# Performance work log

Hardware: AMD Instinct MI355X
Metric: run time of the kernel (lower is better)

The kernel has to match this reference:

```python
import jax, jax.numpy as jnp
import numpy as np

B, S, D, V = 256, 128, 768, 30522
MASK_ID = 103
# vocab ids of the label words (8 positive, 6 neutral, 7 negative)
LABEL_IDS = [
    [2307, 2204, 3835, 2157, 6581, 2986, 5151, 3893],
    [7929, 24791, 8699, 4257, 16021, 6623],
    [6659, 2919, 11771, 3532, 11325, 4997, 13135],
]


def setup_inputs() -> dict:
    key = jax.random.key(0)
    ks = jax.random.split(key, 12)
    length = jax.random.randint(ks[0], (B,), 5, 105)          # 3+length <= 108 < S
    input_ids = jax.random.randint(ks[1], (B, S), 200, 30000)  # never hits MASK_ID
    input_ids = input_ids.at[jnp.arange(B), 3 + length].set(MASK_ID)  # one [MASK] per row
    bert_out = jax.random.normal(ks[2], (B, S, D), dtype=jnp.float32)
    p = lambda k, shp: 0.02 * jax.random.normal(k, shp, dtype=jnp.float32)
    return {
        'bert_out': bert_out,
        'input_ids': input_ids,
        'length': length,
        'senti_w': p(ks[3], (2, D)), 'senti_b': p(ks[4], (2,)),
        'dense_w': p(ks[5], (D, 2 * D)), 'dense_b': p(ks[6], (D,)),
        'dec_w': p(ks[7], (V, D)), 'dec_b': p(ks[8], (V,)),
        'w0': p(ks[9], (2, 8)), 'w1': p(ks[10], (2, 6)), 'w2': p(ks[11], (2, 7)),
    }


def reference(bert_out, input_ids, length, senti_w, senti_b, dense_w, dense_b,
              dec_w, dec_b, w0, w1, w2):
    # pooler -> sentiment head (Dropout is identity at inference)
    pooler = bert_out[:, 0]                                   # [B, D]
    category_out = pooler @ senti_w.T + senti_b               # [B, 2]

    # per-row [MASK] hidden state (exactly one MASK_ID per row)
    mask_pos = jnp.argmax(input_ids == MASK_ID, axis=1)       # [B]
    mask_logits = jnp.take_along_axis(bert_out, mask_pos[:, None, None], axis=1)[:, 0]  # [B, D]

    # attention(): softmax over the ragged slice bert_out[i, 3:3+length[i]]
    scores_raw = jnp.einsum('bsd,bd->bs', bert_out, mask_logits)        # [B, S]
    idx = jnp.arange(S)
    valid = (idx[None, :] >= 3) & (idx[None, :] < 3 + length[:, None])  # [B, S]
    scores = jax.nn.softmax(jnp.where(valid, scores_raw, -jnp.inf), axis=1)
    scores = jnp.where(valid, scores, 0.0)
    att = jnp.einsum('bs,bsd->bd', scores, bert_out)          # [B, D]

    feats = jnp.concatenate([att, mask_logits], axis=1)       # [B, 2D]
    h = jnp.tanh(feats @ dense_w.T + dense_b)                 # [B, D]
    probs = jnp.tanh(h @ dec_w.T + dec_b)                     # [B, V]

    outs = []
    for ids, w in zip(LABEL_IDS, (w0, w1, w2)):
        lp = probs[:, jnp.array(ids)]                         # [B, k]
        outs.append(lp @ w.T)                                 # [B, 2]
    out = jnp.stack(outs, axis=2)                             # [B, 2, 3]
    return category_out, out
```

## Files before the change

kernel.cpp:

```cpp
#include <hip/hip_runtime.h>
#include <hip/hip_bf16.h>
#include <math.h>

#define BB 256
#define SS 128
#define DD 768
#define K2 1536
#define MASK_ID 103

typedef __attribute__((ext_vector_type(8))) short short8;
typedef __attribute__((ext_vector_type(4))) float floatx4;

__constant__ int c_ids[21] = {
    2307, 2204, 3835, 2157, 6581, 2986, 5151, 3893,
    7929, 24791, 8699, 4257, 16021, 6623,
    6659, 2919, 11771, 3532, 11325, 4997, 13135
};

__device__ __forceinline__ float waveReduceSum(float v) {
    #pragma unroll
    for (int off = 32; off > 0; off >>= 1) v += __shfl_down(v, off, 64);
    return v;
}
__device__ __forceinline__ float waveReduceMax(float v) {
    #pragma unroll
    for (int off = 32; off > 0; off >>= 1) v = fmaxf(v, __shfl_down(v, off, 64));
    return v;
}
__device__ __forceinline__ unsigned short f2bf(float f) {
    unsigned int u = __float_as_uint(f);
    u += 0x7FFF + ((u >> 16) & 1);
    return (unsigned short)(u >> 16);
}

__global__ __launch_bounds__(256) void k_cvt(
    const float* __restrict__ src, unsigned short* __restrict__ dst, int n4)
{
    int i = blockIdx.x * 256 + threadIdx.x;
    if (i < n4) {
        float4 v = ((const float4*)src)[i];
        ushort4 o;
        o.x = f2bf(v.x); o.y = f2bf(v.y); o.z = f2bf(v.z); o.w = f2bf(v.w);
        ((ushort4*)dst)[i] = o;
    }
}

__global__ __launch_bounds__(512) void k_att(
    const float* __restrict__ bert, const int* __restrict__ ids,
    const int* __restrict__ len, const float* __restrict__ senti_w,
    const float* __restrict__ senti_b, float* __restrict__ cat_out,
    unsigned short* __restrict__ feats)
{
    __shared__ __align__(16) float s_mask[DD];
    __shared__ __align__(16) float s_part[8][DD];
    __shared__ float s_sc[SS];
    __shared__ float s_red[16];
    __shared__ int s_mp;

    const int b = blockIdx.x;
    const int tid = threadIdx.x;
    const int lane = tid & 63;
    const int wave = tid >> 6;

    if (tid == 0) s_mp = SS;
    __syncthreads();
    if (tid < SS && ids[b * SS + tid] == MASK_ID) atomicMin(&s_mp, tid);
    __syncthreads();
    const int mp = (s_mp == SS) ? 0 : s_mp;
    const int L = len[b];
    const float* base = bert + (size_t)b * SS * DD;
    const float* mrow = base + (size_t)mp * DD;

    float c0 = 0.f, c1 = 0.f;
    for (int d = tid; d < DD; d += 512) {
        s_mask[d] = mrow[d];
        float x = base[d];
        c0 += x * senti_w[d];
        c1 += x * senti_w[DD + d];
    }
    c0 = waveReduceSum(c0);
    c1 = waveReduceSum(c1);
    if (lane == 0) { s_red[wave] = c0; s_red[8 + wave] = c1; }
    __syncthreads();
    if (tid == 0) {
        float t0 = 0.f, t1 = 0.f;
        #pragma unroll
        for (int w = 0; w < 8; ++w) { t0 += s_red[w]; t1 += s_red[8 + w]; }
        cat_out[b * 2 + 0] = t0 + senti_b[0];
        cat_out[b * 2 + 1] = t1 + senti_b[1];
    }

    const float4* m4 = (const float4*)s_mask;
    for (int s = 3 + wave; s < 3 + L; s += 8) {
        const float4* row = (const float4*)(base + (size_t)s * DD);
        float acc = 0.f;
        #pragma unroll
        for (int i = 0; i < 3; ++i) {
            float4 r = row[lane + 64 * i];
            float4 mm = m4[lane + 64 * i];
            acc += r.x * mm.x + r.y * mm.y + r.z * mm.z + r.w * mm.w;
        }
        acc = waveReduceSum(acc);
        if (lane == 0) s_sc[s] = acc;
    }
    __syncthreads();

    const bool valid = (tid >= 3 && tid < 3 + L);
    float v = valid ? s_sc[tid] : -INFINITY;
    float mx = waveReduceMax(v);
    __syncthreads();
    if (lane == 0) s_red[wave] = mx;
    __syncthreads();
    float bm = s_red[0];
    #pragma unroll
    for (int w = 1; w < 8; ++w) bm = fmaxf(bm, s_red[w]);
    float e = valid ? expf(v - bm) : 0.f;
    float ssum = waveReduceSum(e);
    __syncthreads();
    if (lane == 0) s_red[wave] = ssum;
    __syncthreads();
    float tot = 0.f;
    #pragma unroll
    for (int w = 0; w < 8; ++w) tot += s_red[w];
    if (tid < SS) s_sc[tid] = e / tot;
    __syncthreads();

    float4 a0 = {0,0,0,0}, a1 = {0,0,0,0}, a2 = {0,0,0,0};
    for (int s = 3 + wave; s < 3 + L; s += 8) {
        const float w = s_sc[s];
        const float4* row = (const float4*)(base + (size_t)s * DD);
        float4 r0 = row[lane], r1 = row[lane + 64], r2 = row[lane + 128];
        a0.x += w * r0.x; a0.y += w * r0.y; a0.z += w * r0.z; a0.w += w * r0.w;
        a1.x += w * r1.x; a1.y += w * r1.y; a1.z += w * r1.z; a1.w += w * r1.w;
        a2.x += w * r2.x; a2.y += w * r2.y; a2.z += w * r2.z; a2.w += w * r2.w;
    }
    float4* pw = (float4*)s_part[wave];
    pw[lane] = a0; pw[lane + 64] = a1; pw[lane + 128] = a2;
    __syncthreads();

    unsigned short* fb = feats + (size_t)b * K2;
    for (int d = tid; d < DD; d += 512) {
        float a = 0.f;
        #pragma unroll
        for (int w = 0; w < 8; ++w) a += s_part[w][d];
        fb[d] = f2bf(a);
        fb[DD + d] = f2bf(s_mask[d]);
    }
}

__global__ __launch_bounds__(256) void k_dense(
    const unsigned short* __restrict__ featsb,
    const unsigned short* __restrict__ dwb,
    const float* __restrict__ db, float* __restrict__ h)
{
    const int tid = threadIdx.x;
    const int lane = tid & 63, wave = tid >> 6;
    const int b0 = blockIdx.y * 32 + (wave >> 1) * 16;
    const int j0 = blockIdx.x * 32 + (wave & 1) * 16;
    const int m = lane & 15, q = lane >> 4;

    const short8* Arow = (const short8*)(featsb + (size_t)(b0 + m) * K2);
    const short8* Brow = (const short8*)(dwb + (size_t)(j0 + m) * K2);
    floatx4 acc = {0.f, 0.f, 0.f, 0.f};
    #pragma unroll 8
    for (int k8 = 0; k8 < K2 / 8; k8 += 4) {
        short8 a = Arow[k8 + q];
        short8 w = Brow[k8 + q];
        acc = __builtin_amdgcn_mfma_f32_16x16x32_bf16(a, w, acc, 0, 0, 0);
    }
    const int col = j0 + m;
    const int rb = b0 + q * 4;
    const float bias = db[col];
    #pragma unroll
    for (int r = 0; r < 4; ++r)
        h[(size_t)(rb + r) * DD + col] = tanhf(acc[r] + bias);
}

__global__ __launch_bounds__(256) void k_dec(
    const float* __restrict__ h, const float* __restrict__ dec_w,
    const float* __restrict__ dec_b, const float* __restrict__ w0,
    const float* __restrict__ w1, const float* __restrict__ w2,
    float* __restrict__ out)
{
    __shared__ __align__(16) float s_h[DD];
    __shared__ float s_p[21];
    const int b = blockIdx.x;
    const int tid = threadIdx.x;
    const int lane = tid & 63, wave = tid >> 6;

    for (int d = tid; d < DD; d += 256) s_h[d] = h[(size_t)b * DD + d];
    __syncthreads();

    for (int idx = wave; idx < 21; idx += 4) {
        const int vid = c_ids[idx];
        const float* wr = dec_w + (size_t)vid * DD;
        float acc = 0.f;
        #pragma unroll
        for (int i = 0; i < DD / 64; ++i)
            acc += s_h[lane + 64 * i] * wr[lane + 64 * i];
        acc = waveReduceSum(acc);
        if (lane == 0) s_p[idx] = tanhf(acc + dec_b[vid]);
    }
    __syncthreads();

    if (tid < 6) {
        const int c = tid / 3, g = tid % 3;
        const float* wg = (g == 0) ? w0 : (g == 1) ? w1 : w2;
        const int n    = (g == 0) ? 8  : (g == 1) ? 6  : 7;
        const int base = (g == 0) ? 0  : (g == 1) ? 8  : 14;
        float acc = 0.f;
        for (int i = 0; i < n; ++i) acc += s_p[base + i] * wg[c * n + i];
        out[(size_t)b * 6 + c * 3 + g] = acc;
    }
}

extern "C" void kernel_launch(void* const* d_in, const int* in_sizes, int n_in,
                              void* d_out, int out_size, void* d_ws, size_t ws_size,
                              hipStream_t stream) {
    const float* bert    = (const float*)d_in[0];
    const int*   ids     = (const int*)  d_in[1];
    const int*   len     = (const int*)  d_in[2];
    const float* senti_w = (const float*)d_in[3];
    const float* senti_b = (const float*)d_in[4];
    const float* dense_w = (const float*)d_in[5];
    const float* dense_b = (const float*)d_in[6];
    const float* dec_w   = (const float*)d_in[7];
    const float* dec_b   = (const float*)d_in[8];
    const float* w0      = (const float*)d_in[9];
    const float* w1      = (const float*)d_in[10];
    const float* w2      = (const float*)d_in[11];
    float* out = (float*)d_out;

    unsigned short* feats = (unsigned short*)d_ws;
    unsigned short* dwb   = feats + (size_t)BB * K2;
    float* h = (float*)(dwb + (size_t)DD * K2);

    const int n4 = DD * K2 / 4;
    k_cvt<<<(n4 + 255) / 256, 256, 0, stream>>>(dense_w, dwb, n4);
    k_att<<<BB, 512, 0, stream>>>(bert, ids, len, senti_w, senti_b, out, feats);
    k_dense<<<dim3(24, 8), 256, 0, stream>>>(feats, dwb, dense_b, h);
    k_dec<<<BB, 256, 0, stream>>>(h, dec_w, dec_b, w0, w1, w2, out + BB * 2);
}
```

Measured before the change: 230.4 us.

## Fuse attention scores and weighted sum via online softmax in one pass

Replaces the two-pass attention (score pass, block softmax, then weighted-sum pass re-reading bert rows) with a single-pass online softmax per wave. Partial max, sum and accumulators from each wave are merged at the end. The block grows to 1024 threads (16 waves) so more rows are in flight. The aim is to halve the global reads of the ragged rows and remove several block barriers. The cost is extra exp and rescale work per row and a larger shared-memory partial buffer.

```diff
diff --git a/kernel.cpp b/kernel.cpp
--- a/kernel.cpp
+++ b/kernel.cpp
@@ -22,9 +22,9 @@
     for (int off = 32; off > 0; off >>= 1) v += __shfl_down(v, off, 64);
     return v;
 }
-__device__ __forceinline__ float waveReduceMax(float v) {
+__device__ __forceinline__ float waveReduceSumAll(float v) {
     #pragma unroll
-    for (int off = 32; off > 0; off >>= 1) v = fmaxf(v, __shfl_down(v, off, 64));
+    for (int off = 32; off > 0; off >>= 1) v += __shfl_xor(v, off, 64);
     return v;
 }
 __device__ __forceinline__ unsigned short f2bf(float f) {
@@ -45,16 +45,17 @@
     }
 }
 
-__global__ __launch_bounds__(512) void k_att(
+__global__ __launch_bounds__(1024) void k_att(
     const float* __restrict__ bert, const int* __restrict__ ids,
     const int* __restrict__ len, const float* __restrict__ senti_w,
     const float* __restrict__ senti_b, float* __restrict__ cat_out,
     unsigned short* __restrict__ feats)
 {
     __shared__ __align__(16) float s_mask[DD];
-    __shared__ __align__(16) float s_part[8][DD];
-    __shared__ float s_sc[SS];
-    __shared__ float s_red[16];
+    __shared__ __align__(16) float s_part[16][DD];
+    __shared__ float s_m[16], s_l[16], s_scale[16];
+    __shared__ float s_red[32];
+    __shared__ float s_M;
     __shared__ int s_mp;
 
     const int b = blockIdx.x;
@@ -72,79 +73,72 @@
     const float* mrow = base + (size_t)mp * DD;
 
     float c0 = 0.f, c1 = 0.f;
-    for (int d = tid; d < DD; d += 512) {
-        s_mask[d] = mrow[d];
-        float x = base[d];
-        c0 += x * senti_w[d];
-        c1 += x * senti_w[DD + d];
+    if (tid < DD) {
+        s_mask[tid] = mrow[tid];
+        float x = base[tid];
+        c0 = x * senti_w[tid];
+        c1 = x * senti_w[DD + tid];
     }
     c0 = waveReduceSum(c0);
     c1 = waveReduceSum(c1);
-    if (lane == 0) { s_red[wave] = c0; s_red[8 + wave] = c1; }
+    if (lane == 0) { s_red[wave] = c0; s_red[16 + wave] = c1; }
     __syncthreads();
     if (tid == 0) {
         float t0 = 0.f, t1 = 0.f;
         #pragma unroll
-        for (int w = 0; w < 8; ++w) { t0 += s_red[w]; t1 += s_red[8 + w]; }
+        for (int w = 0; w < 16; ++w) { t0 += s_red[w]; t1 += s_red[16 + w]; }
         cat_out[b * 2 + 0] = t0 + senti_b[0];
         cat_out[b * 2 + 1] = t1 + senti_b[1];
     }
 
     const float4* m4 = (const float4*)s_mask;
-    for (int s = 3 + wave; s < 3 + L; s += 8) {
-        const float4* row = (const float4*)(base + (size_t)s * DD);
-        float acc = 0.f;
-        #pragma unroll
-        for (int i = 0; i < 3; ++i) {
-            float4 r = row[lane + 64 * i];
-            float4 mm = m4[lane + 64 * i];
-            acc += r.x * mm.x + r.y * mm.y + r.z * mm.z + r.w * mm.w;
-        }
-        acc = waveReduceSum(acc);
-        if (lane == 0) s_sc[s] = acc;
-    }
-    __syncthreads();
-
-    const bool valid = (tid >= 3 && tid < 3 + L);
-    float v = valid ? s_sc[tid] : -INFINITY;
-    float mx = waveReduceMax(v);
-    __syncthreads();
-    if (lane == 0) s_red[wave] = mx;
-    __syncthreads();
-    float bm = s_red[0];
-    #pragma unroll
-    for (int w = 1; w < 8; ++w) bm = fmaxf(bm, s_red[w]);
-    float e = valid ? expf(v - bm) : 0.f;
-    float ssum = waveReduceSum(e);
-    __syncthreads();
-    if (lane == 0) s_red[wave] = ssum;
-    __syncthreads();
-    float tot = 0.f;
-    #pragma unroll
-    for (int w = 0; w < 8; ++w) tot += s_red[w];
-    if (tid < SS) s_sc[tid] = e / tot;
-    __syncthreads();
-
-    float4 a0 = {0,0,0,0}, a1 = {0,0,0,0}, a2 = {0,0,0,0};
-    for (int s = 3 + wave; s < 3 + L; s += 8) {
-        const float w = s_sc[s];
+    float4 mm0 = m4[lane], mm1 = m4[lane + 64], mm2 = m4[lane + 128];
+    float4 A0 = {0,0,0,0}, A1 = {0,0,0,0}, A2 = {0,0,0,0};
+    float mloc = -INFINITY, lloc = 0.f;
+    for (int s = 3 + wave; s < 3 + L; s += 16) {
         const float4* row = (const float4*)(base + (size_t)s * DD);
         float4 r0 = row[lane], r1 = row[lane + 64], r2 = row[lane + 128];
-        a0.x += w * r0.x; a0.y += w * r0.y; a0.z += w * r0.z; a0.w += w * r0.w;
-        a1.x += w * r1.x; a1.y += w * r1.y; a1.z += w * r1.z; a1.w += w * r1.w;
-        a2.x += w * r2.x; a2.y += w * r2.y; a2.z += w * r2.z; a2.w += w * r2.w;
-    }
+        float d = r0.x * mm0.x + r0.y * mm0.y + r0.z * mm0.z + r0.w * mm0.w
+                + r1.x * mm1.x + r1.y * mm1.y + r1.z * mm1.z + r1.w * mm1.w
+                + r2.x * mm2.x + r2.y * mm2.y + r2.z * mm2.z + r2.w * mm2.w;
+        d = waveReduceSumAll(d);
+        float mnew = fmaxf(mloc, d);
+        float scale = __expf(mloc - mnew);
+        float p = __expf(d - mnew);
+        lloc = lloc * scale + p;
+        A0.x = A0.x * scale + p * r0.x; A0.y = A0.y * scale + p * r0.y;
+        A0.z = A0.z * scale + p * r0.z; A0.w = A0.w * scale + p * r0.w;
+        A1.x = A1.x * scale + p * r1.x; A1.y = A1.y * scale + p * r1.y;
+        A1.z = A1.z * scale + p * r1.z; A1.w = A1.w * scale + p * r1.w;
+        A2.x = A2.x * scale + p * r2.x; A2.y = A2.y * scale + p * r2.y;
+        A2.z = A2.z * scale + p * r2.z; A2.w = A2.w * scale + p * r2.w;
+        mloc = mnew;
+    }
+    if (lane == 0) { s_m[wave] = mloc; s_l[wave] = lloc; }
     float4* pw = (float4*)s_part[wave];
-    pw[lane] = a0; pw[lane + 64] = a1; pw[lane + 128] = a2;
-    __syncthreads();
-
-    unsigned short* fb = feats + (size_t)b * K2;
-    for (int d = tid; d < DD; d += 512) {
-        float a = 0.f;
-        #pragma unroll
-        for (int w = 0; w < 8; ++w) a += s_part[w][d];
-        fb[d] = f2bf(a);
-        fb[DD + d] = f2bf(s_mask[d]);
+    pw[lane] = A0; pw[lane + 64] = A1; pw[lane + 128] = A2;
+    __syncthreads();
+
+    if (tid == 0) {
+        float M = -INFINITY;
+        #pragma unroll
+        for (int w = 0; w < 16; ++w) M = fmaxf(M, s_m[w]);
+        s_M = M;
+    }
+    __syncthreads();
+    if (tid < 16) s_scale[tid] = __expf(s_m[tid] - s_M);
+    __syncthreads();
+
+    if (tid < DD) {
+        float lt = 0.f, a = 0.f;
+        #pragma unroll
+        for (int w = 0; w < 16; ++w) {
+            lt += s_scale[w] * s_l[w];
+            a  += s_scale[w] * s_part[w][tid];
+        }
+        unsigned short* fb = feats + (size_t)b * K2;
+        fb[tid]      = f2bf(a / lt);
+        fb[DD + tid] = f2bf(s_mask[tid]);
     }
 }
 
@@ -237,7 +231,7 @@
 
     const int n4 = DD * K2 / 4;
     k_cvt<<<(n4 + 255) / 256, 256, 0, stream>>>(dense_w, dwb, n4);
-    k_att<<<BB, 512, 0, stream>>>(bert, ids, len, senti_w, senti_b, out, feats);
+    k_att<<<BB, 1024, 0, stream>>>(bert, ids, len, senti_w, senti_b, out, feats);
     k_dense<<<dim3(24, 8), 256, 0, stream>>>(feats, dwb, dense_b, h);
     k_dec<<<BB, 256, 0, stream>>>(h, dec_w, dec_b, w0, w1, w2, out + BB * 2);
 }
```

Result: faster. 224.4 us (-2.6%).
